# Kernel optimization log

Hardware: AMD Instinct MI355X
Metric: run time of the kernel (lower is better)

Reference implementation:

```python
import jax, jax.numpy as jnp
import numpy as np

N_CODES = 1024
CODE_DIM = 256
DECAY = 0.99
EPS = 1e-05


def setup_inputs() -> dict:
    key = jax.random.key(0)
    k1, k2, k3, k4 = jax.random.split(key, 4)
    z = jax.random.normal(k1, (32, CODE_DIM, 32, 32), dtype=jnp.float32)
    embed = jax.random.normal(k2, (N_CODES, CODE_DIM), dtype=jnp.float32)
    cluster_size = jax.random.uniform(k3, (N_CODES,), dtype=jnp.float32)
    embed_avg = jax.random.normal(k4, (N_CODES, CODE_DIM), dtype=jnp.float32)
    return {"z": z, "embed": embed, "cluster_size": cluster_size, "embed_avg": embed_avg}


def reference(z, embed, cluster_size, embed_avg):
    B, D, H, W = z.shape
    K = embed.shape[0]
    # (B*H*W, D) tokens
    flat = jnp.transpose(z, (0, 2, 3, 1)).reshape(-1, D)
    distances = (
        jnp.sum(flat * flat, axis=1, keepdims=True)
        - 2.0 * flat @ embed.T
        + jnp.sum(embed * embed, axis=1)[None, :]
    )
    indices = jnp.argmin(distances, axis=1)  # (N,)
    z_q = embed[indices].reshape(B, H, W, D).transpose(0, 3, 1, 2)  # (B, D, H, W)

    # EMA codebook update (training mode), no onehot materialization
    cs = jax.ops.segment_sum(jnp.ones(flat.shape[0], dtype=flat.dtype), indices, num_segments=K)
    es = jax.ops.segment_sum(flat, indices, num_segments=K)
    new_cluster_size = cluster_size * DECAY + (1.0 - DECAY) * cs
    new_embed_avg = embed_avg * DECAY + (1.0 - DECAY) * es
    n = jnp.sum(new_cluster_size)
    cs_norm = (new_cluster_size + EPS) / (n + K * EPS) * n
    new_embed = new_embed_avg / cs_norm[:, None]

    # straight-through estimator
    z_q_st = z + jax.lax.stop_gradient(z_q - z)
    # torch: F.mse_loss(z.detach(), z_q) -> grads flow to z_q (codebook) only
    vq_loss = jnp.mean((jax.lax.stop_gradient(z) - z_q) ** 2)
    return (z_q_st, indices.reshape(B, H, W), vq_loss, new_embed, new_cluster_size, new_embed_avg)
```

## Files before the change

kernel.cpp:

```cpp
#include <hip/hip_runtime.h>
#include <stdint.h>

#define DECAY 0.99f
#define OMDECAY 0.01f
#define EPSV 1e-5f


typedef _Float16 half8 __attribute__((ext_vector_type(8)));
typedef float floatx4 __attribute__((ext_vector_type(4)));

typedef __attribute__((address_space(1))) const uint32_t gu32;
typedef __attribute__((address_space(3))) uint32_t lu32;

__device__ __forceinline__ void gld16(uint32_t* l, const uint32_t* g) {
    __builtin_amdgcn_global_load_lds((gu32*)g, (lu32*)l, 16, 0, 0);
}

__device__ __forceinline__ uint32_t pack_hl(float v) {
    _Float16 h = (_Float16)v;
    _Float16 lo = (_Float16)(v - (float)h);
    return (uint32_t)__builtin_bit_cast(unsigned short, h) |
           ((uint32_t)__builtin_bit_cast(unsigned short, lo) << 16);
}

__global__ void prep_embed(const float* __restrict__ embed,
                           unsigned short* __restrict__ B_hi16,
                           unsigned short* __restrict__ B_lo16,
                           float* __restrict__ enorm,
                           float* __restrict__ cs ) {
    __shared__ float ws4[4];
    const int k = blockIdx.x;
    const int tid = threadIdx.x;
    const int lane = tid & 63;
    const int wv = tid >> 6;
    int idx = k * 256 + tid;
    float v = embed[idx];
    _Float16 h = (_Float16)v;
    _Float16 lo = (_Float16)(v - (float)h);
    B_hi16[idx] = __builtin_bit_cast(unsigned short, h);
    B_lo16[idx] = __builtin_bit_cast(unsigned short, lo);
    float s = v * v;
    for (int off = 32; off > 0; off >>= 1) s += __shfl_down(s, off);
    if (lane == 0) ws4[wv] = s;
    __syncthreads();
    if (tid == 0) enorm[k] = ws4[0] + ws4[1] + ws4[2] + ws4[3];
    if (k == 0) {
        for (int i = tid; i < 2048; i += 256) cs[i] = 0.f;
    }
}

__global__ void split_z(const float* __restrict__ z,
                        uint32_t* __restrict__ A_hi32,
                        uint32_t* __restrict__ A_lo32) {
    __shared__ uint32_t sp[32 * 258];
    const int lane = threadIdx.x & 63;
    const int wv   = threadIdx.x >> 6;
    const int t0   = blockIdx.x * 32;
    const int b    = t0 >> 10;
    const int hw0  = t0 & 1023;
    const int l32  = lane & 31;
    const int dh   = lane >> 5;

    for (int dp = wv; dp < 128; dp += 4) {
        int dd = dp * 2 + dh;
        float v = z[b * 262144 + dd * 1024 + hw0 + l32];
        sp[l32 * 258 + dd] = pack_hl(v);
    }
    __syncthreads();
    for (int r = wv; r < 32; r += 4) {
#pragma unroll
        for (int h2 = 0; h2 < 2; ++h2) {
            int dpair = h2 * 64 + lane;
            uint32_t u0 = sp[r * 258 + 2 * dpair];
            uint32_t u1 = sp[r * 258 + 2 * dpair + 1];
            A_hi32[(t0 + r) * 128 + dpair] = (u0 & 0xffffu) | (u1 << 16);
            A_lo32[(t0 + r) * 128 + dpair] = (u0 >> 16) | (u1 & 0xffff0000u);
        }
    }
}

__global__ __launch_bounds__(256, 1) void vq_mfma(
    const float* __restrict__ z,
    const float* __restrict__ embed,
    const uint32_t* __restrict__ A_hi32,
    const uint32_t* __restrict__ A_lo32,
    const uint32_t* __restrict__ B_hi32,
    const uint32_t* __restrict__ B_lo32,
    const float* __restrict__ enorm,
    float* __restrict__ out_zq,
    float* __restrict__ out_idx,
    float* __restrict__ cs,
    float* __restrict__ loss_sum)
{
    __shared__ __align__(16) _Float16 AsH[128 * 32];
    __shared__ __align__(16) _Float16 AsL[128 * 32];
    __shared__ __align__(16) _Float16 BsH[256 * 32];
    __shared__ __align__(16) _Float16 BsL[256 * 32];
    __shared__ float smv[512];
    __shared__ int   smi[512];
    __shared__ int   sidx[128];

    const int lane = threadIdx.x & 63;
    const int w    = threadIdx.x >> 6;
    const int q    = lane >> 4;
    const int c16  = lane & 15;
    const int t0   = blockIdx.x * 128;
    const int lane4 = lane >> 2;
    const int dd8   = (lane & 3) * 8;

    float bestv[32];
    int   besti[32];
#pragma unroll
    for (int s = 0; s < 32; ++s) { bestv[s] = 3.4e38f; besti[s] = 0; }

    for (int nc = 0; nc < 4; ++nc) {
        floatx4 acc[8][4];
#pragma unroll
        for (int i = 0; i < 8; ++i)
#pragma unroll
            for (int j = 0; j < 4; ++j)
                acc[i][j] = (floatx4){0.f, 0.f, 0.f, 0.f};

        for (int dc = 0; dc < 8; ++dc) {
            const int d0 = dc * 32;
            __syncthreads();
            for (int s = w; s < 48; s += 4) {
                if (s < 16) {
                    int ss = s & 7;
                    const uint32_t* base = (s < 8) ? A_hi32 : A_lo32;
                    uint32_t* dst = (uint32_t*)((s < 8) ? AsH : AsL) + ss * 256;
                    int tok = ss * 16 + lane4;
                    gld16(dst, base + (t0 + tok) * 128 + ((d0 + dd8) >> 1));
                } else {
                    int sb = s - 16;
                    int ss = sb & 15;
                    const uint32_t* base = (sb < 16) ? B_hi32 : B_lo32;
                    uint32_t* dst = (uint32_t*)((sb < 16) ? BsH : BsL) + ss * 256;
                    int code = nc * 256 + ss * 16 + lane4;
                    gld16(dst, base + code * 128 + ((d0 + dd8) >> 1));
                }
            }
            __syncthreads();

            half8 bH[4], bL[4];
#pragma unroll
            for (int j = 0; j < 4; ++j) {
                int off = (w * 64 + j * 16 + c16) * 32 + q * 8;
                bH[j] = *(const half8*)(BsH + off);
                bL[j] = *(const half8*)(BsL + off);
            }
#pragma unroll
            for (int i = 0; i < 8; ++i) {
                int off = (i * 16 + c16) * 32 + q * 8;
                half8 aH = *(const half8*)(AsH + off);
                half8 aL = *(const half8*)(AsL + off);
#pragma unroll
                for (int j = 0; j < 4; ++j) {
                    acc[i][j] = __builtin_amdgcn_mfma_f32_16x16x32_f16(aH, bH[j], acc[i][j], 0, 0, 0);
                    acc[i][j] = __builtin_amdgcn_mfma_f32_16x16x32_f16(aH, bL[j], acc[i][j], 0, 0, 0);
                    acc[i][j] = __builtin_amdgcn_mfma_f32_16x16x32_f16(aL, bH[j], acc[i][j], 0, 0, 0);
                }
            }
        }

#pragma unroll
        for (int j = 0; j < 4; ++j) {
            int code = nc * 256 + w * 64 + j * 16 + c16;
            float en = enorm[code];
#pragma unroll
            for (int i = 0; i < 8; ++i)
#pragma unroll
                for (int r = 0; r < 4; ++r) {
                    float sc = en - 2.0f * acc[i][j][r];
                    int slot = i * 4 + r;
                    if (sc < bestv[slot] || (sc == bestv[slot] && code < besti[slot])) {
                        bestv[slot] = sc; besti[slot] = code;
                    }
                }
        }
    }

#pragma unroll
    for (int slot = 0; slot < 32; ++slot) {
        float v = bestv[slot]; int bi = besti[slot];
#pragma unroll
        for (int m = 1; m < 16; m <<= 1) {
            float ov = __shfl_xor(v, m);
            int   oi = __shfl_xor(bi, m);
            if (ov < v || (ov == v && oi < bi)) { v = ov; bi = oi; }
        }
        bestv[slot] = v; besti[slot] = bi;
    }
    if (c16 == 0) {
#pragma unroll
        for (int i = 0; i < 8; ++i)
#pragma unroll
            for (int r = 0; r < 4; ++r) {
                int ltok = i * 16 + q * 4 + r;
                smv[w * 128 + ltok] = bestv[i * 4 + r];
                smi[w * 128 + ltok] = besti[i * 4 + r];
            }
    }
    __syncthreads();

    if (threadIdx.x < 128) {
        float bv = smv[threadIdx.x];
        int   bi = smi[threadIdx.x];
#pragma unroll
        for (int ww = 1; ww < 4; ++ww) {
            float v  = smv[ww * 128 + threadIdx.x];
            int   ii = smi[ww * 128 + threadIdx.x];
            if (v < bv || (v == bv && ii < bi)) { bv = v; bi = ii; }
        }
        sidx[threadIdx.x] = bi;
        out_idx[t0 + threadIdx.x] = (float)bi;
        atomicAdd(&cs[bi], 1.0f);
    }
    __syncthreads();

    const int b_idx = t0 >> 10;
    const int hw0   = t0 & 1023;
    const int zbase = b_idx * 262144 + hw0;
    const int ka = sidx[lane];
    const int kb = sidx[lane + 64];
    float lsum = 0.f;
    for (int d = w; d < 256; d += 4) {
        float zv0 = z[zbase + d * 1024 + lane];
        float zv1 = z[zbase + d * 1024 + lane + 64];
        float e0 = embed[ka * 256 + d];
        float e1 = embed[kb * 256 + d];
        out_zq[zbase + d * 1024 + lane]      = zv0 + (e0 - zv0);
        out_zq[zbase + d * 1024 + lane + 64] = zv1 + (e1 - zv1);
        float d0f = zv0 - e0, d1f = zv1 - e1;
        lsum += d0f * d0f + d1f * d1f;
    }
    for (int off = 32; off > 0; off >>= 1) lsum += __shfl_down(lsum, off);
    if (lane == 0) atomicAdd(loss_sum, lsum);
}

__global__ void vq_finalize_small(const float* __restrict__ cluster_size,
                                  const float* __restrict__ cs,
                                  const float* __restrict__ loss_sum,
                                  float* __restrict__ out_loss,
                                  float* __restrict__ out_ncs,
                                  float* __restrict__ csnorm,
                                  int* __restrict__ offsets,
                                  int* __restrict__ cursor)
{
    __shared__ float wsum[16];
    __shared__ float wncs[16];
    __shared__ float stot[1];
    const int k = threadIdx.x;
    const int lane = k & 63;
    const int wv = k >> 6;
    float cnt = cs[k];
    float ncs = cluster_size[k] * DECAY + OMDECAY * cnt;
    out_ncs[k] = ncs;
    float sc = cnt;
#pragma unroll
    for (int d = 1; d < 64; d <<= 1) {
        float up = __shfl_up(sc, d);
        if (lane >= d) sc += up;
    }
    if (lane == 63) wsum[wv] = sc;
    float ns = ncs;
    for (int off = 32; off > 0; off >>= 1) ns += __shfl_down(ns, off);
    if (lane == 0) wncs[wv] = ns;
    __syncthreads();
    if (wv == 0) {
        float v = (lane < 16) ? wsum[lane] : 0.f;
#pragma unroll
        for (int d = 1; d < 16; d <<= 1) {
            float up = __shfl_up(v, d);
            if (lane >= d) v += up;
        }
        if (lane < 16) wsum[lane] = v;
    } else if (wv == 1) {
        float t = (lane < 16) ? wncs[lane] : 0.f;
        for (int off = 32; off > 0; off >>= 1) t += __shfl_down(t, off);
        if (lane == 0) stot[0] = t;
    }
    __syncthreads();
    float incl = sc + (wv ? wsum[wv - 1] : 0.f);
    int excl = __float2int_rn(incl - cnt);
    offsets[k] = excl;
    cursor[k]  = excl;
    float n = stot[0];
    csnorm[k] = (ncs + EPSV) / (n + 1024.0f * EPSV) * n;
    if (k == 0) out_loss[0] = loss_sum[0] / 8388608.0f;
}

__global__ void scatter_perm(const float* __restrict__ out_idx,
                             int* __restrict__ cursor,
                             int* __restrict__ perm,
                             float* __restrict__ es)
{
    int t = blockIdx.x * 256 + threadIdx.x;
#pragma unroll
    for (int i = 0; i < 8; ++i) es[t + i * 32768] = 0.f;
    int code = (int)out_idx[t];
    int pos = atomicAdd(&cursor[code], 1);
    perm[pos] = t;
}

__global__ void es_sum(const uint32_t* __restrict__ A_hi32,
                       const uint32_t* __restrict__ A_lo32,
                       const int* __restrict__ perm,
                       const float* __restrict__ out_idx,
                       float* __restrict__ es)
{
    __shared__ int sperm[32];
    __shared__ int scode[32];
    const int base = blockIdx.x * 32;
    const int tid = threadIdx.x;
    const int j = tid & 127;
    const uint32_t* __restrict__ A = (tid >> 7) ? A_lo32 : A_hi32;
    if (tid < 32) {
        int t = perm[base + tid];
        sperm[tid] = t;
        scode[tid] = (int)out_idx[t];
    }
    __syncthreads();

    float s0 = 0.f, s1 = 0.f;
    int cur = scode[0];
    uint32_t pu[2];
    pu[0] = A[sperm[0] * 128 + j];
    pu[1] = A[sperm[1] * 128 + j];
#pragma unroll
    for (int i = 0; i < 32; ++i) {
        uint32_t u = pu[i & 1];
        if (i + 2 < 32) pu[i & 1] = A[sperm[i + 2] * 128 + j];
        int code = scode[i];
        if (code != cur) {
            atomicAdd(&es[cur * 256 + 2 * j],     s0);
            atomicAdd(&es[cur * 256 + 2 * j + 1], s1);
            s0 = 0.f; s1 = 0.f; cur = code;
        }
        s0 += (float)__builtin_bit_cast(_Float16, (unsigned short)(u & 0xffffu));
        s1 += (float)__builtin_bit_cast(_Float16, (unsigned short)(u >> 16));
    }
    atomicAdd(&es[cur * 256 + 2 * j],     s0);
    atomicAdd(&es[cur * 256 + 2 * j + 1], s1);
}

__global__ void finalize_embed(const float* __restrict__ embed_avg,
                               const float* __restrict__ es,
                               const float* __restrict__ csnorm,
                               float* __restrict__ out_embed,
                               float* __restrict__ out_nea)
{
    int idx = blockIdx.x * 256 + threadIdx.x;
    int k = idx >> 8;
    float nea = embed_avg[idx] * DECAY + OMDECAY * es[idx];
    out_nea[idx] = nea;
    out_embed[idx] = nea / csnorm[k];
}

extern "C" void kernel_launch(void* const* d_in, const int* in_sizes, int n_in,
                              void* d_out, int out_size, void* d_ws, size_t ws_size,
                              hipStream_t stream) {
    const float* z            = (const float*)d_in[0];
    const float* embed        = (const float*)d_in[1];
    const float* cluster_size = (const float*)d_in[2];
    const float* embed_avg    = (const float*)d_in[3];
    float* out = (float*)d_out;
    uint32_t* ws32 = (uint32_t*)d_ws;

    uint32_t* B_hi32 = ws32 + 0;
    uint32_t* B_lo32 = ws32 + 131072;
    uint32_t* A_hi32 = ws32 + 262144;
    uint32_t* A_lo32 = ws32 + 4456448;
    int* perm        = (int*)(ws32 + 8650752);
    int* offsets     = (int*)(ws32 + 8683520);
    int* cursor      = (int*)(ws32 + 8684544);
    float* cs        = (float*)(ws32 + 8912896);
    float* loss_sum  = (float*)(ws32 + 8913920);
    float* enorm     = (float*)(ws32 + 8914944);
    float* csnorm    = (float*)(ws32 + 8915968);
    float* es        = (float*)(ws32 + 0);

    prep_embed<<<1024, 256, 0, stream>>>(embed, (unsigned short*)B_hi32,
                                         (unsigned short*)B_lo32, enorm, cs);
    split_z<<<1024, 256, 0, stream>>>(z, A_hi32, A_lo32);
    vq_mfma<<<256, 256, 0, stream>>>(z, embed, A_hi32, A_lo32, B_hi32, B_lo32, enorm,
                                     out, out + 8388608, cs, loss_sum);
    vq_finalize_small<<<1, 1024, 0, stream>>>(cluster_size, cs, loss_sum,
                                              out + 8421376, out + 8683521, csnorm,
                                              offsets, cursor);
    scatter_perm<<<128, 256, 0, stream>>>(out + 8388608, cursor, perm, es);
    es_sum<<<1024, 256, 0, stream>>>(A_hi32, A_lo32, perm, out + 8388608, es);
    finalize_embed<<<1024, 256, 0, stream>>>(embed_avg, es, csnorm,
                                             out + 8421377, out + 8684545);
}
```

Measured before the change: 278.9 us.

## Split codebook search across two blocks per token tile with 64-bit atomicMin merge

```diff
diff --git a/kernel.cpp b/kernel.cpp
--- a/kernel.cpp
+++ b/kernel.cpp
@@ -23,11 +23,17 @@
            ((uint32_t)__builtin_bit_cast(unsigned short, lo) << 16);
 }
 
+__device__ __forceinline__ unsigned int encf(float s) {
+    unsigned int b = __builtin_bit_cast(unsigned int, s);
+    return (b & 0x80000000u) ? ~b : (b | 0x80000000u);
+}
+
 __global__ void prep_embed(const float* __restrict__ embed,
                            unsigned short* __restrict__ B_hi16,
                            unsigned short* __restrict__ B_lo16,
                            float* __restrict__ enorm,
-                           float* __restrict__ cs ) {
+                           float* __restrict__ cs ,
+                           uint32_t* __restrict__ b64i) {
     __shared__ float ws4[4];
     const int k = blockIdx.x;
     const int tid = threadIdx.x;
@@ -44,6 +50,7 @@
     if (lane == 0) ws4[wv] = s;
     __syncthreads();
     if (tid == 0) enorm[k] = ws4[0] + ws4[1] + ws4[2] + ws4[3];
+    if (k < 256) b64i[k * 256 + tid] = 0xFFFFFFFFu;
     if (k == 0) {
         for (int i = tid; i < 2048; i += 256) cs[i] = 0.f;
     }
@@ -79,41 +86,29 @@
     }
 }
 
-__global__ __launch_bounds__(256, 1) void vq_mfma(
-    const float* __restrict__ z,
-    const float* __restrict__ embed,
+__global__ __launch_bounds__(256, 2) void vq_mfma(
     const uint32_t* __restrict__ A_hi32,
     const uint32_t* __restrict__ A_lo32,
     const uint32_t* __restrict__ B_hi32,
     const uint32_t* __restrict__ B_lo32,
     const float* __restrict__ enorm,
-    float* __restrict__ out_zq,
-    float* __restrict__ out_idx,
-    float* __restrict__ cs,
-    float* __restrict__ loss_sum)
+    unsigned long long* __restrict__ best64)
 {
     __shared__ __align__(16) _Float16 AsH[128 * 32];
     __shared__ __align__(16) _Float16 AsL[128 * 32];
     __shared__ __align__(16) _Float16 BsH[256 * 32];
     __shared__ __align__(16) _Float16 BsL[256 * 32];
-    __shared__ float smv[512];
-    __shared__ int   smi[512];
-    __shared__ int   sidx[128];
 
     const int lane = threadIdx.x & 63;
     const int w    = threadIdx.x >> 6;
     const int q    = lane >> 4;
     const int c16  = lane & 15;
-    const int t0   = blockIdx.x * 128;
+    const int t0   = (blockIdx.x >> 1) * 128;
+    const int cb   = (blockIdx.x & 1) * 512;
     const int lane4 = lane >> 2;
     const int dd8   = (lane & 3) * 8;
 
-    float bestv[32];
-    int   besti[32];
-#pragma unroll
-    for (int s = 0; s < 32; ++s) { bestv[s] = 3.4e38f; besti[s] = 0; }
-
-    for (int nc = 0; nc < 4; ++nc) {
+    for (int nc = 0; nc < 2; ++nc) {
         floatx4 acc[8][4];
 #pragma unroll
         for (int i = 0; i < 8; ++i)
@@ -136,7 +131,7 @@
                     int ss = sb & 15;
                     const uint32_t* base = (sb < 16) ? B_hi32 : B_lo32;
                     uint32_t* dst = (uint32_t*)((sb < 16) ? BsH : BsL) + ss * 256;
-                    int code = nc * 256 + ss * 16 + lane4;
+                    int code = cb + nc * 256 + ss * 16 + lane4;
                     gld16(dst, base + code * 128 + ((d0 + dd8) >> 1));
                 }
             }
@@ -163,9 +158,13 @@
             }
         }
 
+        float bestv[32];
+        int   besti[32];
+#pragma unroll
+        for (int s = 0; s < 32; ++s) { bestv[s] = 3.4e38f; besti[s] = 0; }
 #pragma unroll
         for (int j = 0; j < 4; ++j) {
-            int code = nc * 256 + w * 64 + j * 16 + c16;
+            int code = cb + nc * 256 + w * 64 + j * 16 + c16;
             float en = enorm[code];
 #pragma unroll
             for (int i = 0; i < 8; ++i)
@@ -178,42 +177,49 @@
                     }
                 }
         }
-    }
-
-#pragma unroll
-    for (int slot = 0; slot < 32; ++slot) {
-        float v = bestv[slot]; int bi = besti[slot];
-#pragma unroll
-        for (int m = 1; m < 16; m <<= 1) {
-            float ov = __shfl_xor(v, m);
-            int   oi = __shfl_xor(bi, m);
-            if (ov < v || (ov == v && oi < bi)) { v = ov; bi = oi; }
-        }
-        bestv[slot] = v; besti[slot] = bi;
-    }
-    if (c16 == 0) {
-#pragma unroll
-        for (int i = 0; i < 8; ++i)
-#pragma unroll
-            for (int r = 0; r < 4; ++r) {
-                int ltok = i * 16 + q * 4 + r;
-                smv[w * 128 + ltok] = bestv[i * 4 + r];
-                smi[w * 128 + ltok] = besti[i * 4 + r];
+#pragma unroll
+        for (int slot = 0; slot < 32; ++slot) {
+            float v = bestv[slot]; int bi = besti[slot];
+#pragma unroll
+            for (int m = 1; m < 16; m <<= 1) {
+                float ov = __shfl_xor(v, m);
+                int   oi = __shfl_xor(bi, m);
+                if (ov < v || (ov == v && oi < bi)) { v = ov; bi = oi; }
             }
-    }
-    __syncthreads();
-
-    if (threadIdx.x < 128) {
-        float bv = smv[threadIdx.x];
-        int   bi = smi[threadIdx.x];
-#pragma unroll
-        for (int ww = 1; ww < 4; ++ww) {
-            float v  = smv[ww * 128 + threadIdx.x];
-            int   ii = smi[ww * 128 + threadIdx.x];
-            if (v < bv || (v == bv && ii < bi)) { bv = v; bi = ii; }
-        }
-        sidx[threadIdx.x] = bi;
-        out_idx[t0 + threadIdx.x] = (float)bi;
+            bestv[slot] = v; besti[slot] = bi;
+        }
+#pragma unroll
+        for (int slot = 0; slot < 32; ++slot) {
+            if (c16 == (slot & 15)) {
+                int tok = (slot >> 2) * 16 + q * 4 + (slot & 3);
+                unsigned long long key =
+                    ((unsigned long long)encf(bestv[slot]) << 32) |
+                    (unsigned int)besti[slot];
+                atomicMin(&best64[t0 + tok], key);
+            }
+        }
+    }
+}
+
+__global__ __launch_bounds__(256) void merge_zq(
+    const unsigned long long* __restrict__ best64,
+    const float* __restrict__ z,
+    const float* __restrict__ embed,
+    float* __restrict__ out_zq,
+    float* __restrict__ out_idx,
+    float* __restrict__ cs,
+    float* __restrict__ loss_sum)
+{
+    __shared__ int sidx[128];
+    const int tid = threadIdx.x;
+    const int lane = tid & 63;
+    const int w = tid >> 6;
+    const int t0 = blockIdx.x * 128;
+
+    if (tid < 128) {
+        int bi = (int)(unsigned int)(best64[t0 + tid] & 0xffffffffULL);
+        sidx[tid] = bi;
+        out_idx[t0 + tid] = (float)bi;
         atomicAdd(&cs[bi], 1.0f);
     }
     __syncthreads();
@@ -379,12 +385,15 @@
     float* enorm     = (float*)(ws32 + 8914944);
     float* csnorm    = (float*)(ws32 + 8915968);
     float* es        = (float*)(ws32 + 0);
+    unsigned long long* best64 = (unsigned long long*)(out + 8421378);
 
     prep_embed<<<1024, 256, 0, stream>>>(embed, (unsigned short*)B_hi32,
-                                         (unsigned short*)B_lo32, enorm, cs);
+                                         (unsigned short*)B_lo32, enorm, cs,
+                                         (uint32_t*)best64);
     split_z<<<1024, 256, 0, stream>>>(z, A_hi32, A_lo32);
-    vq_mfma<<<256, 256, 0, stream>>>(z, embed, A_hi32, A_lo32, B_hi32, B_lo32, enorm,
-                                     out, out + 8388608, cs, loss_sum);
+    vq_mfma<<<512, 256, 0, stream>>>(A_hi32, A_lo32, B_hi32, B_lo32, enorm, best64);
+    merge_zq<<<256, 256, 0, stream>>>(best64, z, embed,
+                                      out, out + 8388608, cs, loss_sum);
     vq_finalize_small<<<1, 1024, 0, stream>>>(cluster_size, cs, loss_sum,
                                               out + 8421376, out + 8683521, csnorm,
                                               offsets, cursor);
```

Result: faster. 264.4 us (-5.2%).
